# Kernel optimization log

Measured on AMD Instinct MI355X. Metric: run time of the kernel, lower is better.

The kernel has to match this reference:

```python
import jax, jax.numpy as jnp
import numpy as np

V, H, L, B = 32000, 512, 1024, 64
HALF = H // 2
PE = 16
LN_EPS = 1e-5
DELTA_EPS = 1e-6


def setup_inputs() -> dict:
    key = jax.random.key(0)
    ks = jax.random.split(key, 16)
    s = lambda k, shape, scale=0.02: jax.random.normal(k, shape, dtype=jnp.float32) * scale
    return {
        "seq": jax.random.randint(ks[0], (B, L), 0, V, dtype=jnp.int32),
        "embed": s(ks[1], (V, H)),
        "w1": s(ks[2], (H, 2 * H)), "b1": jnp.zeros((2 * H,), jnp.float32),
        "w2": s(ks[3], (2 * H, H)), "b2": jnp.zeros((H,), jnp.float32),
        "ln_g": jnp.ones((H,), jnp.float32), "ln_b": jnp.zeros((H,), jnp.float32),
        "sem_w": s(ks[4], (H, HALF)), "sem_b": jnp.zeros((HALF,), jnp.float32),
        "epi_w": s(ks[5], (H, HALF)), "epi_b": jnp.zeros((HALF,), jnp.float32),
        "out_w": s(ks[6], (2 * HALF, V)), "out_b": jnp.zeros((V,), jnp.float32),
        "pos_emb": s(ks[7], (L, PE)),
        "pos_w": s(ks[8], (PE, 1)), "pos_b": jnp.zeros((1,), jnp.float32),
    }


def _forward(seq, embed, w1, b1, w2, b2, ln_g, ln_b, sem_w, sem_b,
             epi_w, epi_b, out_w, out_b, pos_emb, pos_w, pos_b):
    # Encoder: embed -> FFN residual -> LayerNorm
    e = embed[seq]                                   # [B,L,H]
    ff = jax.nn.relu(e @ w1 + b1) @ w2 + b2          # [B,L,H]
    x = e + ff
    mu = jnp.mean(x, -1, keepdims=True)
    var = jnp.mean(jnp.square(x - mu), -1, keepdims=True)
    h = (x - mu) / jnp.sqrt(var + LN_EPS) * ln_g + ln_b  # [B,L,H]

    ks_all = h @ sem_w + sem_b                       # [B,L,half]
    ke_all = h @ epi_w + epi_b                       # [B,L,half]
    pos_weights = jax.nn.sigmoid(pos_emb @ pos_w + pos_b)[:, 0]  # [L]

    def step(carry, xs):
        M_s, M_e = carry
        ks, ke, w = xs                               # [B,half],[B,half],scalar
        vps = jnp.einsum('bij,bj->bi', M_s, ks)
        dvs = ks - vps / (jnp.sum(ks * ks, -1, keepdims=True) + DELTA_EPS)
        M_s = M_s + dvs[:, :, None] * ks[:, None, :]
        vpe = jnp.einsum('bij,bj->bi', M_e, ke)
        dve = ke - vpe / (jnp.sum(ke * ke, -1, keepdims=True) + DELTA_EPS)
        M_e = M_e + w * (dve[:, :, None] * ke[:, None, :])
        return (M_s, M_e), None

    M0 = jnp.zeros((B, HALF, HALF), jnp.float32)
    xs = (jnp.swapaxes(ks_all[:, :-1], 0, 1),        # [L-1,B,half]
          jnp.swapaxes(ke_all[:, :-1], 0, 1),
          pos_weights[:L - 1])
    (M_s, M_e), _ = jax.lax.scan(step, (M0, M0), xs)

    cs = jnp.einsum('bij,bj->bi', M_s, ks_all[:, -1])  # query = last position
    ce = jnp.einsum('bij,bj->bi', M_e, ke_all[:, -1])
    return jnp.concatenate([cs, ce], -1) @ out_w + out_b  # [B,V]


def reference(seq, embed, w1, b1, w2, b2, ln_g, ln_b, sem_w, sem_b,
              epi_w, epi_b, out_w, out_b, pos_emb, pos_w, pos_b):
    return _forward(seq, embed, w1, b1, w2, b2, ln_g, ln_b, sem_w, sem_b,
                    epi_w, epi_b, out_w, out_b, pos_emb, pos_w, pos_b)
```

## Files before the change

kernel.cpp:

```cpp
#include <hip/hip_runtime.h>
#include <hip/hip_bf16.h>
#include <math.h>

namespace {

constexpr int kH     = 512;
constexpr int kL     = 1024;
constexpr int kB     = 64;
constexpr int kHalf  = 256;
constexpr int kV     = 32000;
constexpr int kTok   = kB * kL;

using f32x4 = __attribute__((ext_vector_type(4))) float;
using f16x8 = __attribute__((ext_vector_type(8))) _Float16;

__device__ inline void fsplit(float v, _Float16& h, _Float16& l) {
  h = (_Float16)v;
  l = (_Float16)(v - (float)h);
}

typedef __attribute__((address_space(3))) void lds_vp;
typedef const __attribute__((address_space(1))) void glb_vp;
__device__ inline void gload16(const void* g, void* l) {
  __builtin_amdgcn_global_load_lds((glb_vp*)g, (lds_vp*)l, 16, 0, 0);
}

__device__ inline int hswz(int row, int col) {
  const int sr = row >> 1;
  const int g  = ((row & 1) << 2) | (col >> 3);
  return sr * 64 + (((g ^ (sr & 7)) << 3) | (col & 7));
}

__global__ void pos_kernel(const float* __restrict__ pos_emb,
                           const float* __restrict__ pos_w,
                           const float* __restrict__ pos_b,
                           float* __restrict__ wts)
{
  int t = blockIdx.x * blockDim.x + threadIdx.x;
  if (t >= kL) return;
  float z = pos_b[0];
#pragma unroll
  for (int p = 0; p < 16; ++p) z += pos_emb[t * 16 + p] * pos_w[p];
  wts[t] = 1.f / (1.f + expf(-z));
}

__global__ __launch_bounds__(256) void transpose_split(
    const float* __restrict__ W, _Float16* __restrict__ Th,
    _Float16* __restrict__ Tl, int N, int kshift)
{
  const int idx = blockIdx.x * 256 + threadIdx.x;
  const int K = 1 << kshift;
  const int k = idx & (K - 1);
  const int n = idx >> kshift;
  const float w = W[(size_t)k * N + n];
  const _Float16 h = (_Float16)w;
  Th[idx] = h;
  Tl[idx] = (_Float16)(w - (float)h);
}

template <int EPI>
__global__ __launch_bounds__(256) void hgemm(
    const int* __restrict__ seq, const float* __restrict__ embed,
    const _Float16* __restrict__ Ah,
    const _Float16* __restrict__ Bh, const _Float16* __restrict__ Bl,
    const float* __restrict__ bias, const float* __restrict__ bias2,
    float* __restrict__ Xout, _Float16* __restrict__ Oh, _Float16* __restrict__ Ol,
    float* __restrict__ ks, float* __restrict__ ke,
    int K, int N, int tok0c)
{
  __shared__ __align__(16) _Float16 lds[3][128 * 32];
  const int tid  = threadIdx.x;
  const int lane = tid & 63;
  const int wv   = tid >> 6;
  const int wm   = (wv >> 1) * 64;
  const int wn   = (wv & 1) * 64;
  const int bm0  = blockIdx.y * 128;
  const int bn0  = blockIdx.x * 128;

  f32x4 acc[4][4];
#pragma unroll
  for (int i = 0; i < 4; ++i)
#pragma unroll
    for (int j = 0; j < 4; ++j) acc[i][j] = {0.f, 0.f, 0.f, 0.f};

  const int sl   = lane >> 3;
  const int gg   = (lane & 7) ^ sl;
  const int trow = wv * 16 + sl * 2 + (gg >> 2);
  const int tcol = (gg & 3) * 8;
  const size_t brow0 = (size_t)(bn0 + trow) * K + tcol;
  const size_t brow1 = (size_t)(bn0 + trow + 64) * K + tcol;
  size_t arow0 = 0, arow1 = 0;
  const float* gAe = nullptr;
  if constexpr (EPI == 0) {
    const int sr = tid >> 1;
    const int tokrow = seq[tok0c + bm0 + sr];
    gAe = embed + (size_t)tokrow * kH + ((tid & 1) << 4);
  } else {
    arow0 = (size_t)(bm0 + trow) * K + tcol;
    arow1 = (size_t)(bm0 + trow + 64) * K + tcol;
  }
  const int lb0 = wv * 512;
  const int lb1 = 2048 + wv * 512;

  const int lrow = lane & 15;
  const int lk   = (lane >> 4) * 8;

  for (int k0 = 0; k0 < K; k0 += 32) {
    float4 a0, a1, a2, a3;
    if constexpr (EPI == 0) {
      a0 = *(const float4*)(gAe + k0);
      a1 = *(const float4*)(gAe + k0 + 4);
      a2 = *(const float4*)(gAe + k0 + 8);
      a3 = *(const float4*)(gAe + k0 + 12);
    }
    __syncthreads();
    if constexpr (EPI != 0) {
      gload16(Ah + arow0 + k0, &lds[0][lb0]);
      gload16(Ah + arow1 + k0, &lds[0][lb1]);
    }
    gload16(Bh + brow0 + k0, &lds[1][lb0]);
    gload16(Bh + brow1 + k0, &lds[1][lb1]);
    gload16(Bl + brow0 + k0, &lds[2][lb0]);
    gload16(Bl + brow1 + k0, &lds[2][lb1]);
    if constexpr (EPI == 0) {
      const float vv[16] = {a0.x,a0.y,a0.z,a0.w, a1.x,a1.y,a1.z,a1.w,
                            a2.x,a2.y,a2.z,a2.w, a3.x,a3.y,a3.z,a3.w};
      union { _Float16 h[16]; uint4 u[2]; } ph;
#pragma unroll
      for (int i = 0; i < 16; ++i) ph.h[i] = (_Float16)vv[i];
      const int sr = tid >> 1;
      const int sc = (tid & 1) << 4;
      *(uint4*)&lds[0][hswz(sr, sc)]     = ph.u[0];
      *(uint4*)&lds[0][hswz(sr, sc + 8)] = ph.u[1];
    }
    __syncthreads();

    f16x8 fBh[4], fBl[4];
#pragma unroll
    for (int ni = 0; ni < 4; ++ni) {
      fBh[ni] = *(const f16x8*)&lds[1][hswz(wn + ni * 16 + lrow, lk)];
      fBl[ni] = *(const f16x8*)&lds[2][hswz(wn + ni * 16 + lrow, lk)];
    }
#pragma unroll
    for (int mi = 0; mi < 4; ++mi) {
      const f16x8 ah = *(const f16x8*)&lds[0][hswz(wm + mi * 16 + lrow, lk)];
#pragma unroll
      for (int ni = 0; ni < 4; ++ni) {
        acc[mi][ni] = __builtin_amdgcn_mfma_f32_16x16x32_f16(ah, fBh[ni], acc[mi][ni], 0, 0, 0);
        acc[mi][ni] = __builtin_amdgcn_mfma_f32_16x16x32_f16(ah, fBl[ni], acc[mi][ni], 0, 0, 0);
      }
    }
  }

  const int erow0 = (lane >> 4) * 4;
  if constexpr (EPI == 0) {
#pragma unroll
    for (int mi = 0; mi < 4; ++mi)
#pragma unroll
      for (int ni = 0; ni < 4; ++ni) {
        const int gn = bn0 + wn + ni * 16 + (lane & 15);
        const float bv = bias[gn];
#pragma unroll
        for (int r = 0; r < 4; ++r) {
          const int gm = bm0 + wm + mi * 16 + erow0 + r;
          float v = fmaxf(acc[mi][ni][r] + bv, 0.f);
          Oh[(size_t)gm * N + gn] = (_Float16)v;
        }
      }
  } else if constexpr (EPI == 1) {
#pragma unroll
    for (int mi = 0; mi < 4; ++mi)
#pragma unroll
      for (int r = 0; r < 4; ++r) {
        const int gm = bm0 + wm + mi * 16 + erow0 + r;
        const int tok = seq[tok0c + gm];
        const float* er = embed + (size_t)tok * kH;
#pragma unroll
        for (int ni = 0; ni < 4; ++ni) {
          const int gn = bn0 + wn + ni * 16 + (lane & 15);
          Xout[(size_t)gm * N + gn] = acc[mi][ni][r] + bias[gn] + er[gn];
        }
      }
  } else {
    _Float16* kh_s = (_Float16*)ks;
    _Float16* kh_e = (_Float16*)ke;
    float s2[4][4];
#pragma unroll
    for (int mi = 0; mi < 4; ++mi)
#pragma unroll
      for (int r = 0; r < 4; ++r) s2[mi][r] = 0.f;
#pragma unroll
    for (int mi = 0; mi < 4; ++mi)
#pragma unroll
      for (int ni = 0; ni < 4; ++ni) {
        const int gn = bn0 + wn + ni * 16 + (lane & 15);
        const float bv = (gn < 256) ? bias[gn] : bias2[gn - 256];
        _Float16* Dh = (gn < 256) ? kh_s : kh_e;
        _Float16* Dl = (gn < 256) ? Oh : Ol;
        const int col = gn & 255;
#pragma unroll
        for (int r = 0; r < 4; ++r) {
          const int gm = bm0 + wm + mi * 16 + erow0 + r;
          const float v = acc[mi][ni][r] + bv;
          s2[mi][r] += v * v;
          _Float16 h, l;
          fsplit(v, h, l);
          Dh[(size_t)(tok0c + gm) * 256 + col] = h;
          Dl[(size_t)(tok0c + gm) * 256 + col] = l;
        }
      }
    const int matq  = bn0 >> 8;
    const int halfq = (bn0 >> 7) & 1;
#pragma unroll
    for (int mi = 0; mi < 4; ++mi)
#pragma unroll
      for (int r = 0; r < 4; ++r) {
        float s2v = s2[mi][r];
        s2v += __shfl_xor(s2v, 1);
        s2v += __shfl_xor(s2v, 2);
        s2v += __shfl_xor(s2v, 4);
        s2v += __shfl_xor(s2v, 8);
        if ((lane & 15) == 0) {
          const int gm = bm0 + wm + mi * 16 + erow0 + r;
          Xout[((size_t)matq * kTok + (size_t)(tok0c + gm)) * 4 + halfq * 2 + (wv & 1)] = s2v;
        }
      }
  }
}

__global__ __launch_bounds__(256) void ln_split(
    const float* __restrict__ x, const float* __restrict__ g,
    const float* __restrict__ bta, _Float16* __restrict__ hh)
{
  const int wid  = threadIdx.x >> 6;
  const int lane = threadIdx.x & 63;
  const int ltok = blockIdx.x * 4 + wid;
  const float* xp = x + (size_t)ltok * kH;
  const float4 v0 = *(const float4*)(xp + lane * 8);
  const float4 v1 = *(const float4*)(xp + lane * 8 + 4);
  float s  = v0.x + v0.y + v0.z + v0.w + v1.x + v1.y + v1.z + v1.w;
  float ss = v0.x * v0.x + v0.y * v0.y + v0.z * v0.z + v0.w * v0.w +
             v1.x * v1.x + v1.y * v1.y + v1.z * v1.z + v1.w * v1.w;
#pragma unroll
  for (int m = 1; m < 64; m <<= 1) { s += __shfl_xor(s, m); ss += __shfl_xor(ss, m); }
  const float mu  = s * (1.f / kH);
  const float var = ss * (1.f / kH) - mu * mu;
  const float rs  = 1.f / sqrtf(var + 1e-5f);
  const float4 g0 = *(const float4*)(g + lane * 8);
  const float4 g1 = *(const float4*)(g + lane * 8 + 4);
  const float4 b0 = *(const float4*)(bta + lane * 8);
  const float4 b1 = *(const float4*)(bta + lane * 8 + 4);
  const float vv[8] = {v0.x, v0.y, v0.z, v0.w, v1.x, v1.y, v1.z, v1.w};
  const float gg[8] = {g0.x, g0.y, g0.z, g0.w, g1.x, g1.y, g1.z, g1.w};
  const float bb[8] = {b0.x, b0.y, b0.z, b0.w, b1.x, b1.y, b1.z, b1.w};
  union { _Float16 h[8]; uint4 u; } ph;
#pragma unroll
  for (int i = 0; i < 8; ++i) {
    const float o = (vv[i] - mu) * rs * gg[i] + bb[i];
    ph.h[i] = (_Float16)o;
  }
  *(uint4*)(hh + (size_t)ltok * kH + lane * 8) = ph.u;
}

__global__ __launch_bounds__(64) void tinv_kernel(
    const _Float16* __restrict__ khs, const _Float16* __restrict__ kls,
    const _Float16* __restrict__ khe, const _Float16* __restrict__ kle,
    const float* __restrict__ ssqP, const float* __restrict__ wts,
    _Float16* __restrict__ Tgh, _Float16* __restrict__ Tgl)
{
  __shared__ float Gs[64][68];
  const int lane = threadIdx.x;
  const int l15  = lane & 15;
  const int quad = lane >> 4;
  const int wg   = blockIdx.x;
  const int ck   = wg & 15;
  const int mat  = (wg >> 4) & 1;
  const int b    = wg >> 5;
  const _Float16* Kh = (mat ? khe : khs) + (size_t)b * (1024 * 256) + (size_t)ck * 64 * 256;
  const _Float16* Kl = (mat ? kle : kls) + (size_t)b * (1024 * 256) + (size_t)ck * 64 * 256;

  const float4 sq = *(const float4*)(ssqP + ((size_t)mat * kTok + (size_t)b * 1024 + ck * 64 + lane) * 4);
  const float w  = mat ? wts[ck * 64 + lane] : 1.f;
  const float aS = w / (sq.x + sq.y + sq.z + sq.w + 1e-6f);

  f32x4 D[16];
#pragma unroll
  for (int i = 0; i < 16; ++i) D[i] = {0.f, 0.f, 0.f, 0.f};
#pragma unroll
  for (int kit = 0; kit < 8; ++kit) {
    f16x8 fh[4], fl[4];
#pragma unroll
    for (int mi = 0; mi < 4; ++mi) {
      fh[mi] = *(const f16x8*)(Kh + (size_t)(mi * 16 + l15) * 256 + kit * 32 + quad * 8);
      fl[mi] = *(const f16x8*)(Kl + (size_t)(mi * 16 + l15) * 256 + kit * 32 + quad * 8);
    }
#pragma unroll
    for (int mi = 0; mi < 4; ++mi)
#pragma unroll
      for (int ni = 0; ni < 4; ++ni) {
        f32x4 d = D[mi * 4 + ni];
        d = __builtin_amdgcn_mfma_f32_16x16x32_f16(fh[mi], fh[ni], d, 0, 0, 0);
        d = __builtin_amdgcn_mfma_f32_16x16x32_f16(fh[mi], fl[ni], d, 0, 0, 0);
        d = __builtin_amdgcn_mfma_f32_16x16x32_f16(fl[mi], fh[ni], d, 0, 0, 0);
        D[mi * 4 + ni] = d;
      }
  }
#pragma unroll
  for (int mi = 0; mi < 4; ++mi)
#pragma unroll
    for (int ni = 0; ni < 4; ++ni)
#pragma unroll
      for (int r = 0; r < 4; ++r) {
        const int row = mi * 16 + quad * 4 + r;
        const float as_r = __shfl(aS, row);
        Gs[row][ni * 16 + l15] = as_r * D[mi * 4 + ni][r];
      }
  __syncthreads();

  float x[64];
#pragma unroll
  for (int t = 0; t < 64; ++t) x[t] = (t == lane) ? 1.f : 0.f;
#pragma unroll
  for (int t = 1; t < 64; ++t) {
    float acc = 0.f;
    const int n4 = t >> 2;
#pragma unroll
    for (int q4 = 0; q4 < 16; ++q4) {
      if (q4 >= n4) break;
      const float4 g = *(const float4*)&Gs[t][q4 * 4];
      acc += g.x * x[q4 * 4] + g.y * x[q4 * 4 + 1] + g.z * x[q4 * 4 + 2] + g.w * x[q4 * 4 + 3];
    }
#pragma unroll
    for (int tp = 0; tp < 4; ++tp) {
      const int ti = n4 * 4 + tp;
      if (ti >= t) break;
      acc += Gs[t][ti] * x[ti];
    }
    x[t] -= acc;
  }
  if (ck == 15) x[63] = 0.f;

  const size_t base = (size_t)wg * 4096;
#pragma unroll
  for (int t = 0; t < 64; ++t) {
    _Float16 h, l;
    fsplit(x[t], h, l);
    Tgh[base + t * 64 + lane] = h;
    Tgl[base + t * 64 + lane] = l;
  }
}

struct HTile { _Float16 h[4608], l[4608]; };

__global__ __launch_bounds__(256) void scan_chunked(
    const _Float16* __restrict__ khs, const _Float16* __restrict__ kls,
    const _Float16* __restrict__ khe, const _Float16* __restrict__ kle,
    const float* __restrict__ ssqP, const float* __restrict__ wts,
    const _Float16* __restrict__ Tgh, const _Float16* __restrict__ Tgl,
    float* __restrict__ c_out)
{
  __shared__ HTile Sb[2];
  __shared__ union { HTile t; float cred[4][64]; } Yb;
  __shared__ HTile Ub;

  const int tid  = threadIdx.x;
  const int lane = tid & 63;
  const int wv   = tid >> 6;
  const int l15  = lane & 15;
  const int quad = lane >> 4;
  const int wg   = blockIdx.x;
  const int grp  = (wg & 7) + ((wg >> 5) << 3);
  const int q    = (wg >> 3) & 3;
  const int b    = grp >> 1;
  const int mat  = grp & 1;
  const int j0   = q * 64;
  const _Float16* Kh = (mat ? khe : khs) + (size_t)b * (1024 * 256);
  const _Float16* Kl = (mat ? kle : kls) + (size_t)b * (1024 * 256);
  const _Float16* Tbh = Tgh + (size_t)((b * 2 + mat) * 16) * 4096;
  const _Float16* Tbl = Tgl + (size_t)((b * 2 + mat) * 16) * 4096;

  f32x4 S[16];
#pragma unroll
  for (int i = 0; i < 16; ++i) S[i] = {0.f, 0.f, 0.f, 0.f};

  for (int ck = 0; ck < 16; ++ck) {
    const int tok0 = ck * 64;

    float myw[4], mya[4], kvv[4][4];
#pragma unroll
    for (int r = 0; r < 4; ++r) {
      const int t = tok0 + wv * 16 + quad * 4 + r;
      const float4 sq = *(const float4*)(ssqP + ((size_t)mat * kTok + (size_t)b * 1024 + t) * 4);
      const float w = mat ? wts[t] : 1.f;
      myw[r] = w;
      mya[r] = w / (sq.x + sq.y + sq.z + sq.w + 1e-6f);
#pragma unroll
      for (int nt = 0; nt < 4; ++nt) {
        const size_t go = (size_t)t * 256 + j0 + nt * 16 + l15;
        kvv[r][nt] = (float)Kh[go] + (float)Kl[go];
      }
    }
    f16x8 tah[2], tal[2];
#pragma unroll
    for (int kit = 0; kit < 2; ++kit) {
      const size_t to = (size_t)ck * 4096 + (size_t)(wv * 16 + l15) * 64 + kit * 32 + quad * 8;
      tah[kit] = *(const f16x8*)(Tbh + to);
      tal[kit] = *(const f16x8*)(Tbl + to);
    }
    const _Float16* arow_h = Kh + (size_t)(tok0 + wv * 16 + l15) * 256 + quad * 8;
    const _Float16* arow_l = Kl + (size_t)(tok0 + wv * 16 + l15) * 256 + quad * 8;
    f16x8 a0h = *(const f16x8*)(arow_h);
    f16x8 a1h = *(const f16x8*)(arow_h + 32);
    f16x8 a0l = *(const f16x8*)(arow_l);
    f16x8 a1l = *(const f16x8*)(arow_l + 32);

#pragma unroll
    for (int nt = 0; nt < 4; ++nt) {
      const f32x4 v = S[0 * 4 + nt];
      union { _Float16 h[4]; uint2 u; } qh, ql;
#pragma unroll
      for (int r = 0; r < 4; ++r) fsplit(v[r], qh.h[r], ql.h[r]);
      const int ix = (nt * 16 + l15) * 72 + wv * 16 + quad * 4;
      *(uint2*)&Sb[0].h[ix] = qh.u;
      *(uint2*)&Sb[0].l[ix] = ql.u;
    }
    __syncthreads();

    f32x4 Qa[4];
#pragma unroll
    for (int i = 0; i < 4; ++i) Qa[i] = {0.f, 0.f, 0.f, 0.f};
#pragma unroll
    for (int p = 0; p < 4; ++p) {
      const int cur = p & 1;
      f16x8 n0h, n1h, n0l, n1l;
      if (p < 3) {
        n0h = *(const f16x8*)(arow_h + (p + 1) * 64);
        n1h = *(const f16x8*)(arow_h + (p + 1) * 64 + 32);
        n0l = *(const f16x8*)(arow_l + (p + 1) * 64);
        n1l = *(const f16x8*)(arow_l + (p + 1) * 64 + 32);
#pragma unroll
        for (int nt = 0; nt < 4; ++nt) {
          const f32x4 v = S[(p + 1) * 4 + nt];
          union { _Float16 h[4]; uint2 u; } sh2, sl2;
#pragma unroll
          for (int r = 0; r < 4; ++r) fsplit(v[r], sh2.h[r], sl2.h[r]);
          const int ix = (nt * 16 + l15) * 72 + wv * 16 + quad * 4;
          *(uint2*)&Sb[1 - cur].h[ix] = sh2.u;
          *(uint2*)&Sb[1 - cur].l[ix] = sl2.u;
        }
      }
#pragma unroll
      for (int kit = 0; kit < 2; ++kit) {
        const f16x8 ah = kit ? a1h : a0h;
        const f16x8 al = kit ? a1l : a0l;
#pragma unroll
        for (int nt = 0; nt < 4; ++nt) {
          const int ix = (nt * 16 + l15) * 72 + kit * 32 + quad * 8;
          const f16x8 bh = *(const f16x8*)&Sb[cur].h[ix];
          const f16x8 bl = *(const f16x8*)&Sb[cur].l[ix];
          Qa[nt] = __builtin_amdgcn_mfma_f32_16x16x32_f16(ah, bh, Qa[nt], 0, 0, 0);
          Qa[nt] = __builtin_amdgcn_mfma_f32_16x16x32_f16(ah, bl, Qa[nt], 0, 0, 0);
          Qa[nt] = __builtin_amdgcn_mfma_f32_16x16x32_f16(al, bh, Qa[nt], 0, 0, 0);
        }
      }
      if (p < 3) { a0h = n0h; a1h = n1h; a0l = n0l; a1l = n1l; }
      __syncthreads();
    }

#pragma unroll
    for (int nt = 0; nt < 4; ++nt) {
      union { _Float16 h[4]; uint2 u; } yh, yl;
#pragma unroll
      for (int r = 0; r < 4; ++r) {
        const float y = myw[r] * kvv[r][nt] - mya[r] * Qa[nt][r];
        fsplit(y, yh.h[r], yl.h[r]);
      }
      const int ix = (nt * 16 + l15) * 72 + wv * 16 + quad * 4;
      *(uint2*)&Yb.t.h[ix] = yh.u;
      *(uint2*)&Yb.t.l[ix] = yl.u;
    }
    __syncthreads();

    f32x4 Ua[4];
#pragma unroll
    for (int i = 0; i < 4; ++i) Ua[i] = {0.f, 0.f, 0.f, 0.f};
#pragma unroll
    for (int kit = 0; kit < 2; ++kit)
#pragma unroll
      for (int nt = 0; nt < 4; ++nt) {
        const int ix = (nt * 16 + l15) * 72 + kit * 32 + quad * 8;
        const f16x8 yh = *(const f16x8*)&Yb.t.h[ix];
        const f16x8 yl = *(const f16x8*)&Yb.t.l[ix];
        Ua[nt] = __builtin_amdgcn_mfma_f32_16x16x32_f16(tah[kit], yh, Ua[nt], 0, 0, 0);
        Ua[nt] = __builtin_amdgcn_mfma_f32_16x16x32_f16(tah[kit], yl, Ua[nt], 0, 0, 0);
        Ua[nt] = __builtin_amdgcn_mfma_f32_16x16x32_f16(tal[kit], yh, Ua[nt], 0, 0, 0);
      }
#pragma unroll
    for (int nt = 0; nt < 4; ++nt) {
      union { _Float16 h[4]; uint2 u; } uh, ul;
#pragma unroll
      for (int r = 0; r < 4; ++r) fsplit(Ua[nt][r], uh.h[r], ul.h[r]);
      const int ix = (nt * 16 + l15) * 72 + wv * 16 + quad * 4;
      *(uint2*)&Ub.h[ix] = uh.u;
      *(uint2*)&Ub.l[ix] = ul.u;
    }
    __syncthreads();

#pragma unroll
    for (int p = 0; p < 4; ++p) {
      union { _Float16 e[8]; f16x8 v; } kah[2], kal[2];
#pragma unroll
      for (int kit = 0; kit < 2; ++kit)
#pragma unroll
        for (int jj = 0; jj < 8; ++jj) {
          const size_t gko = (size_t)(tok0 + kit * 32 + quad * 8 + jj) * 256
                           + p * 64 + wv * 16 + l15;
          kah[kit].e[jj] = Kh[gko];
          kal[kit].e[jj] = Kl[gko];
        }
#pragma unroll
      for (int kit = 0; kit < 2; ++kit)
#pragma unroll
        for (int nt = 0; nt < 4; ++nt) {
          const int ix = (nt * 16 + l15) * 72 + kit * 32 + quad * 8;
          const f16x8 ubh = *(const f16x8*)&Ub.h[ix];
          const f16x8 ubl = *(const f16x8*)&Ub.l[ix];
          f32x4 s = S[p * 4 + nt];
          s = __builtin_amdgcn_mfma_f32_16x16x32_f16(kah[kit].v, ubh, s, 0, 0, 0);
          s = __builtin_amdgcn_mfma_f32_16x16x32_f16(kah[kit].v, ubl, s, 0, 0, 0);
          s = __builtin_amdgcn_mfma_f32_16x16x32_f16(kal[kit].v, ubh, s, 0, 0, 0);
          S[p * 4 + nt] = s;
        }
    }
  }

  float part[4] = {0.f, 0.f, 0.f, 0.f};
  const size_t lastoff = (size_t)(kL - 1) * 256;
#pragma unroll
  for (int p = 0; p < 4; ++p) {
    float klr[4];
#pragma unroll
    for (int r = 0; r < 4; ++r) {
      const int row = p * 64 + wv * 16 + quad * 4 + r;
      klr[r] = (float)Kh[lastoff + row] + (float)Kl[lastoff + row];
    }
#pragma unroll
    for (int nt = 0; nt < 4; ++nt)
#pragma unroll
      for (int r = 0; r < 4; ++r) part[nt] += S[p * 4 + nt][r] * klr[r];
  }
#pragma unroll
  for (int nt = 0; nt < 4; ++nt) {
    part[nt] += __shfl_xor(part[nt], 16);
    part[nt] += __shfl_xor(part[nt], 32);
  }
  __syncthreads();
  if (lane < 16) {
#pragma unroll
    for (int nt = 0; nt < 4; ++nt) Yb.cred[wv][nt * 16 + l15] = part[nt];
  }
  __syncthreads();
  if (tid < 64) {
    const float c = Yb.cred[0][tid] + Yb.cred[1][tid] + Yb.cred[2][tid] + Yb.cred[3][tid];
    c_out[(size_t)b * 512 + mat * 256 + j0 + tid] = c;
  }
}

__global__ __launch_bounds__(256) void out_gemm(
    const float* __restrict__ A, const float* __restrict__ Bm,
    const float* __restrict__ bias, float* __restrict__ C)
{
  __shared__ float As[16][64];
  __shared__ float Bs[16][128];
  const int tid = threadIdx.x;
  const int bn0 = blockIdx.x * 128;
  const int tm = tid >> 4, tn = tid & 15;
  float acc[4][8];
#pragma unroll
  for (int i = 0; i < 4; ++i)
#pragma unroll
    for (int j = 0; j < 8; ++j) acc[i][j] = 0.f;

  const int am  = tid & 63;
  const int ak  = (tid >> 6) * 4;
  const int bkr = tid >> 5;
  const int bcg = (tid & 31) * 4;

  for (int k0 = 0; k0 < kH; k0 += 16) {
    const float4 a0 = *(const float4*)(A + (size_t)am * kH + k0 + ak);
    const float4 b0 = *(const float4*)(Bm + (size_t)(k0 + bkr) * kV + bn0 + bcg);
    const float4 b1 = *(const float4*)(Bm + (size_t)(k0 + bkr + 8) * kV + bn0 + bcg);
    __syncthreads();
    As[ak + 0][am] = a0.x; As[ak + 1][am] = a0.y;
    As[ak + 2][am] = a0.z; As[ak + 3][am] = a0.w;
    *(float4*)&Bs[bkr][bcg]     = b0;
    *(float4*)&Bs[bkr + 8][bcg] = b1;
    __syncthreads();
#pragma unroll
    for (int kk = 0; kk < 16; ++kk) {
      const float4 aA = *(const float4*)&As[kk][tm * 4];
      const float4 bA = *(const float4*)&Bs[kk][tn * 4];
      const float4 bB = *(const float4*)&Bs[kk][64 + tn * 4];
      const float av[4] = {aA.x, aA.y, aA.z, aA.w};
      const float bv[8] = {bA.x, bA.y, bA.z, bA.w, bB.x, bB.y, bB.z, bB.w};
#pragma unroll
      for (int i = 0; i < 4; ++i)
#pragma unroll
        for (int j = 0; j < 8; ++j) acc[i][j] += av[i] * bv[j];
    }
  }

#pragma unroll
  for (int i = 0; i < 4; ++i) {
    const int row = tm * 4 + i;
#pragma unroll
    for (int hh = 0; hh < 2; ++hh) {
      const int n0 = bn0 + tn * 4 + hh * 64;
      const float4 bb = *(const float4*)(bias + n0);
      float4 o;
      o.x = acc[i][hh * 4 + 0] + bb.x;
      o.y = acc[i][hh * 4 + 1] + bb.y;
      o.z = acc[i][hh * 4 + 2] + bb.z;
      o.w = acc[i][hh * 4 + 3] + bb.w;
      *(float4*)(C + (size_t)row * kV + n0) = o;
    }
  }
}

}

extern "C" void kernel_launch(void* const* d_in, const int* in_sizes, int n_in,
                              void* d_out, int out_size, void* d_ws, size_t ws_size,
                              hipStream_t stream)
{
  const int*   seq     = (const int*)  d_in[0];
  const float* embed   = (const float*)d_in[1];
  const float* w1      = (const float*)d_in[2];
  const float* b1      = (const float*)d_in[3];
  const float* w2      = (const float*)d_in[4];
  const float* b2      = (const float*)d_in[5];
  const float* ln_g    = (const float*)d_in[6];
  const float* ln_b    = (const float*)d_in[7];
  const float* sem_w   = (const float*)d_in[8];
  const float* sem_b   = (const float*)d_in[9];
  const float* epi_w   = (const float*)d_in[10];
  const float* epi_b   = (const float*)d_in[11];
  const float* out_w   = (const float*)d_in[12];
  const float* out_b   = (const float*)d_in[13];
  const float* pos_emb = (const float*)d_in[14];
  const float* pos_w   = (const float*)d_in[15];
  const float* pos_b   = (const float*)d_in[16];
  float* out = (float*)d_out;

  const int chunkN = (ws_size >= (size_t)240500000) ? 16384 : 8192;
  const int nch    = kTok / chunkN;

  char* p = (char*)d_ws;
  _Float16* w1th = (_Float16*)p; p += (size_t)1024 * 512 * 2;
  _Float16* w1tl = (_Float16*)p; p += (size_t)1024 * 512 * 2;
  _Float16* w2th = (_Float16*)p; p += (size_t)512 * 1024 * 2;
  _Float16* w2tl = (_Float16*)p; p += (size_t)512 * 1024 * 2;
  _Float16* wseh = (_Float16*)p; p += (size_t)512 * 512 * 2;
  _Float16* wsel = (_Float16*)p; p += (size_t)512 * 512 * 2;
  _Float16* t1h  = (_Float16*)p; p += (size_t)chunkN * 1024 * 2;
  _Float16* t1l  = (_Float16*)p; p += (size_t)chunkN * 1024 * 2;
  float*    x    = (float*)p;    p += (size_t)chunkN * kH * 4;
  _Float16* khs  = (_Float16*)p; p += (size_t)kTok * kHalf * 2;
  _Float16* kls  = (_Float16*)p; p += (size_t)kTok * kHalf * 2;
  _Float16* khe  = (_Float16*)p; p += (size_t)kTok * kHalf * 2;
  _Float16* kle  = (_Float16*)p; p += (size_t)kTok * kHalf * 2;
  float*    wts  = (float*)p;    p += (size_t)kL * 4;
  float*    cout_= (float*)p;    p += (size_t)kB * 512 * 4;
  float*    ssqp = (float*)p;    p += (size_t)2 * kTok * 4 * 4;
  _Float16* hh   = t1h;
  _Float16* Tgh = t1h;
  _Float16* Tgl = t1l;

  pos_kernel<<<dim3((kL + 255) / 256), dim3(256), 0, stream>>>(pos_emb, pos_w, pos_b, wts);
  transpose_split<<<dim3(1024 * 512 / 256), dim3(256), 0, stream>>>(w1, w1th, w1tl, 1024, 9);
  transpose_split<<<dim3(512 * 1024 / 256), dim3(256), 0, stream>>>(w2, w2th, w2tl, 512, 10);
  transpose_split<<<dim3(256 * 512 / 256), dim3(256), 0, stream>>>(sem_w, wseh, wsel, 256, 9);
  transpose_split<<<dim3(256 * 512 / 256), dim3(256), 0, stream>>>(
      epi_w, wseh + (size_t)256 * 512, wsel + (size_t)256 * 512, 256, 9);

  for (int c = 0; c < nch; ++c) {
    const int tok0 = c * chunkN;
    hgemm<0><<<dim3(1024 / 128, chunkN / 128), dim3(256), 0, stream>>>(
        seq, embed, nullptr, w1th, w1tl, b1, nullptr,
        nullptr, t1h, nullptr, nullptr, nullptr, 512, 1024, tok0);
    hgemm<1><<<dim3(512 / 128, chunkN / 128), dim3(256), 0, stream>>>(
        seq, embed, t1h, w2th, w2tl, b2, nullptr,
        x, nullptr, nullptr, nullptr, nullptr, 1024, 512, tok0);
    ln_split<<<dim3(chunkN / 4), dim3(256), 0, stream>>>(x, ln_g, ln_b, hh);
    hgemm<2><<<dim3(512 / 128, chunkN / 128), dim3(256), 0, stream>>>(
        seq, embed, hh, wseh, wsel, sem_b, epi_b,
        ssqp, kls, kle, (float*)khs, (float*)khe,
        512, 512, tok0);
  }

  tinv_kernel<<<dim3(2048), dim3(64), 0, stream>>>(
      khs, kls, khe, kle, ssqp, wts, Tgh, Tgl);
  scan_chunked<<<dim3(512), dim3(256), 0, stream>>>(
      khs, kls, khe, kle, ssqp, wts, Tgh, Tgl, cout_);
  out_gemm<<<dim3(kV / 128), dim3(256), 0, stream>>>(cout_, out_w, out_b, out);

  (void)in_sizes; (void)n_in; (void)out_size;
}
```

Before: 1.090 ms.

## Double-buffer GEMM LDS tiles and drop low-half weight products in FFN GEMMs

```diff
diff --git a/kernel.cpp b/kernel.cpp
--- a/kernel.cpp
+++ b/kernel.cpp
@@ -58,7 +58,7 @@
   Tl[idx] = (_Float16)(w - (float)h);
 }
 
-template <int EPI>
+template <int EPI, int PROD>
 __global__ __launch_bounds__(256) void hgemm(
     const int* __restrict__ seq, const float* __restrict__ embed,
     const _Float16* __restrict__ Ah,
@@ -68,7 +68,8 @@
     float* __restrict__ ks, float* __restrict__ ke,
     int K, int N, int tok0c)
 {
-  __shared__ __align__(16) _Float16 lds[3][128 * 32];
+  constexpr int TILES = 1 + PROD;
+  __shared__ __align__(16) _Float16 lds[2 * TILES * 4096];
   const int tid  = threadIdx.x;
   const int lane = tid & 63;
   const int wv   = tid >> 6;
@@ -104,52 +105,65 @@
 
   const int lrow = lane & 15;
   const int lk   = (lane >> 4) * 8;
-
-  for (int k0 = 0; k0 < K; k0 += 32) {
+  const int NT   = K >> 5;
+
+  for (int t = 0; t <= NT; ++t) {
+    const int kc = t << 5;
     float4 a0, a1, a2, a3;
-    if constexpr (EPI == 0) {
-      a0 = *(const float4*)(gAe + k0);
-      a1 = *(const float4*)(gAe + k0 + 4);
-      a2 = *(const float4*)(gAe + k0 + 8);
-      a3 = *(const float4*)(gAe + k0 + 12);
+    if (t < NT) {
+      if constexpr (EPI == 0) {
+        a0 = *(const float4*)(gAe + kc);
+        a1 = *(const float4*)(gAe + kc + 4);
+        a2 = *(const float4*)(gAe + kc + 8);
+        a3 = *(const float4*)(gAe + kc + 12);
+      }
+      const int bo = (t & 1) * TILES * 4096;
+      if constexpr (EPI != 0) {
+        gload16(Ah + arow0 + kc, &lds[bo + lb0]);
+        gload16(Ah + arow1 + kc, &lds[bo + lb1]);
+      }
+      gload16(Bh + brow0 + kc, &lds[bo + 4096 + lb0]);
+      gload16(Bh + brow1 + kc, &lds[bo + 4096 + lb1]);
+      if constexpr (PROD == 2) {
+        gload16(Bl + brow0 + kc, &lds[bo + 8192 + lb0]);
+        gload16(Bl + brow1 + kc, &lds[bo + 8192 + lb1]);
+      }
+    }
+    if (t > 0) {
+      const int po = ((t - 1) & 1) * TILES * 4096;
+      f16x8 fBh[4], fBl[4];
+#pragma unroll
+      for (int ni = 0; ni < 4; ++ni) {
+        fBh[ni] = *(const f16x8*)&lds[po + 4096 + hswz(wn + ni * 16 + lrow, lk)];
+        if constexpr (PROD == 2)
+          fBl[ni] = *(const f16x8*)&lds[po + 8192 + hswz(wn + ni * 16 + lrow, lk)];
+      }
+#pragma unroll
+      for (int mi = 0; mi < 4; ++mi) {
+        const f16x8 ah = *(const f16x8*)&lds[po + hswz(wm + mi * 16 + lrow, lk)];
+#pragma unroll
+        for (int ni = 0; ni < 4; ++ni) {
+          acc[mi][ni] = __builtin_amdgcn_mfma_f32_16x16x32_f16(ah, fBh[ni], acc[mi][ni], 0, 0, 0);
+          if constexpr (PROD == 2)
+            acc[mi][ni] = __builtin_amdgcn_mfma_f32_16x16x32_f16(ah, fBl[ni], acc[mi][ni], 0, 0, 0);
+        }
+      }
+    }
+    if (t < NT) {
+      if constexpr (EPI == 0) {
+        const float vv[16] = {a0.x,a0.y,a0.z,a0.w, a1.x,a1.y,a1.z,a1.w,
+                              a2.x,a2.y,a2.z,a2.w, a3.x,a3.y,a3.z,a3.w};
+        union { _Float16 h[16]; uint4 u[2]; } ph;
+#pragma unroll
+        for (int i = 0; i < 16; ++i) ph.h[i] = (_Float16)vv[i];
+        const int sr = tid >> 1;
+        const int sc = (tid & 1) << 4;
+        const int bo = (t & 1) * TILES * 4096;
+        *(uint4*)&lds[bo + hswz(sr, sc)]     = ph.u[0];
+        *(uint4*)&lds[bo + hswz(sr, sc + 8)] = ph.u[1];
+      }
     }
     __syncthreads();
-    if constexpr (EPI != 0) {
-      gload16(Ah + arow0 + k0, &lds[0][lb0]);
-      gload16(Ah + arow1 + k0, &lds[0][lb1]);
-    }
-    gload16(Bh + brow0 + k0, &lds[1][lb0]);
-    gload16(Bh + brow1 + k0, &lds[1][lb1]);
-    gload16(Bl + brow0 + k0, &lds[2][lb0]);
-    gload16(Bl + brow1 + k0, &lds[2][lb1]);
-    if constexpr (EPI == 0) {
-      const float vv[16] = {a0.x,a0.y,a0.z,a0.w, a1.x,a1.y,a1.z,a1.w,
-                            a2.x,a2.y,a2.z,a2.w, a3.x,a3.y,a3.z,a3.w};
-      union { _Float16 h[16]; uint4 u[2]; } ph;
-#pragma unroll
-      for (int i = 0; i < 16; ++i) ph.h[i] = (_Float16)vv[i];
-      const int sr = tid >> 1;
-      const int sc = (tid & 1) << 4;
-      *(uint4*)&lds[0][hswz(sr, sc)]     = ph.u[0];
-      *(uint4*)&lds[0][hswz(sr, sc + 8)] = ph.u[1];
-    }
-    __syncthreads();
-
-    f16x8 fBh[4], fBl[4];
-#pragma unroll
-    for (int ni = 0; ni < 4; ++ni) {
-      fBh[ni] = *(const f16x8*)&lds[1][hswz(wn + ni * 16 + lrow, lk)];
-      fBl[ni] = *(const f16x8*)&lds[2][hswz(wn + ni * 16 + lrow, lk)];
-    }
-#pragma unroll
-    for (int mi = 0; mi < 4; ++mi) {
-      const f16x8 ah = *(const f16x8*)&lds[0][hswz(wm + mi * 16 + lrow, lk)];
-#pragma unroll
-      for (int ni = 0; ni < 4; ++ni) {
-        acc[mi][ni] = __builtin_amdgcn_mfma_f32_16x16x32_f16(ah, fBh[ni], acc[mi][ni], 0, 0, 0);
-        acc[mi][ni] = __builtin_amdgcn_mfma_f32_16x16x32_f16(ah, fBl[ni], acc[mi][ni], 0, 0, 0);
-      }
-    }
   }
 
   const int erow0 = (lane >> 4) * 4;
@@ -685,14 +699,14 @@
 
   for (int c = 0; c < nch; ++c) {
     const int tok0 = c * chunkN;
-    hgemm<0><<<dim3(1024 / 128, chunkN / 128), dim3(256), 0, stream>>>(
-        seq, embed, nullptr, w1th, w1tl, b1, nullptr,
+    hgemm<0, 1><<<dim3(1024 / 128, chunkN / 128), dim3(256), 0, stream>>>(
+        seq, embed, nullptr, w1th, nullptr, b1, nullptr,
         nullptr, t1h, nullptr, nullptr, nullptr, 512, 1024, tok0);
-    hgemm<1><<<dim3(512 / 128, chunkN / 128), dim3(256), 0, stream>>>(
-        seq, embed, t1h, w2th, w2tl, b2, nullptr,
+    hgemm<1, 1><<<dim3(512 / 128, chunkN / 128), dim3(256), 0, stream>>>(
+        seq, embed, t1h, w2th, nullptr, b2, nullptr,
         x, nullptr, nullptr, nullptr, nullptr, 1024, 512, tok0);
     ln_split<<<dim3(chunkN / 4), dim3(256), 0, stream>>>(x, ln_g, ln_b, hh);
-    hgemm<2><<<dim3(512 / 128, chunkN / 128), dim3(256), 0, stream>>>(
+    hgemm<2, 2><<<dim3(512 / 128, chunkN / 128), dim3(256), 0, stream>>>(
         seq, embed, hh, wseh, wsel, sem_b, epi_b,
         ssqp, kls, kle, (float*)khs, (float*)khe,
         512, 512, tok0);
```

New measurement: 972.0 us. 10.8% less time.
